# Performance work log

Measured on AMD Instinct MI355X. Metric: run time of the kernel, lower is better.

The kernel has to match this reference:

```python
import jax, jax.numpy as jnp
import numpy as np

N = 50000       # population nodes
E = 1_600_000   # edges per edge type
F_IN = 2000     # flattened individual-graph embedding (100*20)
D = 20          # hidden channels per TransformerConv head (heads=1)
NEG_SLOPE = 0.01
BN_EPS = 1e-5


def setup_inputs() -> dict:
    key = jax.random.key(0)
    ks = jax.random.split(key, 24)
    features = jax.random.normal(ks[0], (N, F_IN), jnp.float32)
    same_index = jax.random.randint(ks[1], (2, E), 0, N, dtype=jnp.int64)
    diff_index = jax.random.randint(ks[2], (2, E), 0, N, dtype=jnp.int64)
    s0 = 1.0 / np.sqrt(F_IN)
    s1 = 1.0 / np.sqrt(D)
    # layer 0 conv params, stacked over the 2 edge types (same, diff)
    W0q = jax.random.normal(ks[3], (2, F_IN, D), jnp.float32) * s0
    W0k = jax.random.normal(ks[4], (2, F_IN, D), jnp.float32) * s0
    W0v = jax.random.normal(ks[5], (2, F_IN, D), jnp.float32) * s0
    W0s = jax.random.normal(ks[6], (2, F_IN, D), jnp.float32) * s0
    b0q = jnp.zeros((2, D)); b0k = jnp.zeros((2, D))
    b0v = jnp.zeros((2, D)); b0s = jnp.zeros((2, D))
    # layers 1..3 conv params: [layer, edge_type, D, D]
    Wq = jax.random.normal(ks[7], (3, 2, D, D), jnp.float32) * s1
    Wk = jax.random.normal(ks[8], (3, 2, D, D), jnp.float32) * s1
    Wv = jax.random.normal(ks[9], (3, 2, D, D), jnp.float32) * s1
    Ws = jax.random.normal(ks[10], (3, 2, D, D), jnp.float32) * s1
    bq = jnp.zeros((3, 2, D)); bk = jnp.zeros((3, 2, D))
    bv = jnp.zeros((3, 2, D)); bs = jnp.zeros((3, 2, D))
    w1 = jnp.full((4,), 0.8, jnp.float32)
    w2 = jnp.full((4,), 0.2, jnp.float32)
    bn_gamma = jnp.ones((4, D), jnp.float32)
    bn_beta = jnp.zeros((4, D), jnp.float32)
    Wout = jax.random.normal(ks[11], (4 * D, 2), jnp.float32) / np.sqrt(4 * D)
    bout = jnp.zeros((2,), jnp.float32)
    return dict(features=features, same_index=same_index, diff_index=diff_index,
                W0q=W0q, b0q=b0q, W0k=W0k, b0k=b0k, W0v=W0v, b0v=b0v, W0s=W0s, b0s=b0s,
                Wq=Wq, bq=bq, Wk=Wk, bk=bk, Wv=Wv, bv=bv, Ws=Ws, bs=bs,
                w1=w1, w2=w2, bn_gamma=bn_gamma, bn_beta=bn_beta, Wout=Wout, bout=bout)


def _tconv(x, edge_index, Wq, bq, Wk, bk, Wv, bv, Ws, bs):
    """PyG TransformerConv, heads=1, concat=True, root_weight=True, no edge_attr."""
    src, dst = edge_index[0], edge_index[1]
    q = x @ Wq + bq   # [N, D]
    k = x @ Wk + bk
    v = x @ Wv + bv
    logits = jnp.einsum('ed,ed->e', q[dst], k[src]) / jnp.sqrt(jnp.float32(D))  # [E]
    m = jax.ops.segment_max(logits, dst, num_segments=N)
    m = jnp.where(jnp.isfinite(m), m, jnp.float32(0.0))  # nodes with no in-edges
    e = jnp.exp(logits - m[dst])
    z = jax.ops.segment_sum(e, dst, num_segments=N)
    alpha = e / (z[dst] + 1e-16)  # PyG softmax epsilon
    agg = jax.ops.segment_sum(alpha[:, None] * v[src], dst, num_segments=N)  # [N, D]
    return agg + x @ Ws + bs  # skip (root) connection


def _bn(x, gamma, beta):
    mu = x.mean(axis=0)
    var = x.var(axis=0)
    return (x - mu) * jax.lax.rsqrt(var + BN_EPS) * gamma + beta


def reference(features, same_index, diff_index,
              W0q, b0q, W0k, b0k, W0v, b0v, W0s, b0s,
              Wq, bq, Wk, bk, Wv, bv, Ws, bs,
              w1, w2, bn_gamma, bn_beta, Wout, bout):
    x = features
    fcs = []
    for l in range(4):
        if l == 0:
            p_same = (W0q[0], b0q[0], W0k[0], b0k[0], W0v[0], b0v[0], W0s[0], b0s[0])
            p_diff = (W0q[1], b0q[1], W0k[1], b0k[1], W0v[1], b0v[1], W0s[1], b0s[1])
        else:
            i = l - 1
            p_same = (Wq[i, 0], bq[i, 0], Wk[i, 0], bk[i, 0], Wv[i, 0], bv[i, 0], Ws[i, 0], bs[i, 0])
            p_diff = (Wq[i, 1], bq[i, 1], Wk[i, 1], bk[i, 1], Wv[i, 1], bv[i, 1], Ws[i, 1], bs[i, 1])
        x1 = _tconv(x, same_index, *p_same)
        x2 = _tconv(x, diff_index, *p_diff)
        t = w1[l] + w2[l]
        x = (w1[l] / t) * x1 + (w2[l] / t) * x2
        x = _bn(x, bn_gamma[l], bn_beta[l])
        x = jax.nn.leaky_relu(x, NEG_SLOPE)
        fcs.append(x)
    fc = jnp.concatenate(fcs, axis=-1)  # [N, 80]
    return fc @ Wout + bout  # [N, 2]
```

## Files before the change

kernel.cpp:

```cpp
#include <hip/hip_runtime.h>
#include <math.h>

#define N_NODES 50000
#define E_EDGES 1600000
#define F_IN    2000
#define D       20
#define NCOL    160
#define KPAD    2016
#define NBNP    64

#define INV_SQRT_D 0.22360679774997896f

typedef __bf16 bf16x8 __attribute__((ext_vector_type(8)));
typedef __bf16 bf16x4 __attribute__((ext_vector_type(4)));
typedef float  f32x4  __attribute__((ext_vector_type(4)));


__global__ void pack_kernel(
    const float* __restrict__ W0q, const float* __restrict__ W0k,
    const float* __restrict__ W0v, const float* __restrict__ W0s,
    const float* __restrict__ b0q, const float* __restrict__ b0k,
    const float* __restrict__ b0v, const float* __restrict__ b0s,
    const float* __restrict__ Wq,  const float* __restrict__ Wk,
    const float* __restrict__ Wv,  const float* __restrict__ Ws_,
    const float* __restrict__ bq,  const float* __restrict__ bk,
    const float* __restrict__ bv,  const float* __restrict__ bs_,
    __bf16* __restrict__ B0, float* __restrict__ bias0,
    float* __restrict__ WL, float* __restrict__ biasL,
    float* __restrict__ bnp, int* __restrict__ deg)
{
  long idx = (long)blockIdx.x * blockDim.x + threadIdx.x;
  if (idx < (long)NCOL*KPAD) {
    int col = (int)(idx / KPAD), k = (int)(idx % KPAD);
    int et = col / 80, r = col % 80, mat = r / 20, d = r % 20;
    const float* w = (mat==0)?W0q:(mat==1)?W0s:(mat==2)?W0k:W0v;
    float v = (k < F_IN) ? w[((size_t)et*F_IN + k)*D + d] : 0.f;
    B0[idx] = (__bf16)v;
    return;
  }
  idx -= (long)NCOL*KPAD;
  if (idx < 160) {
    int col = (int)idx;
    int et = col / 80, r = col % 80, mat = r / 20, d = r % 20;
    const float* b = (mat==0)?b0q:(mat==1)?b0s:(mat==2)?b0k:b0v;
    bias0[col] = b[et*D + d];
    return;
  }
  idx -= 160;
  if (idx < 9600) {
    int l = (int)(idx / 3200), rem = (int)(idx % 3200);
    int k = rem / NCOL, col = rem % NCOL;
    int et = col / 80, r = col % 80, mat = r / 20, d = r % 20;
    const float* w = (mat==0)?Wq:(mat==1)?Ws_:(mat==2)?Wk:Wv;
    WL[idx] = w[(((size_t)l*2 + et)*D + k)*D + d];
    return;
  }
  idx -= 9600;
  if (idx < 480) {
    int l = (int)(idx / NCOL), col = (int)(idx % NCOL);
    int et = col / 80, r = col % 80, mat = r / 20, d = r % 20;
    const float* b = (mat==0)?bq:(mat==1)?bs_:(mat==2)?bk:bv;
    biasL[idx] = b[(l*2 + et)*D + d];
    return;
  }
  idx -= 480;
  if (idx < 4*NBNP*40) { bnp[idx] = 0.f; return; }
  idx -= 4*NBNP*40;
  if (idx < 2*N_NODES) { deg[idx] = 0; return; }
}

#define SC_EPT 16
#define SC_CHUNK (256*SC_EPT)

__global__ void hist_kernel(const int* __restrict__ same, const int* __restrict__ diff,
                            int* __restrict__ deg)
{
  const int part  = blockIdx.x & 7;
  const int chunk = blockIdx.x >> 3;
  const int lo = part * (N_NODES/8);
  const int hi = lo + (N_NODES/8);
  const long i0 = (long)chunk * SC_CHUNK + threadIdx.x;
#pragma unroll
  for (int it = 0; it < SC_EPT; ++it) {
    long i = i0 + (long)it*256;
    if (i >= 2L*E_EDGES) break;
    int et = (i >= E_EDGES) ? 1 : 0;
    long e = i - (long)et*E_EDGES;
    const int* ix = et ? diff : same;
    int dst = ix[E_EDGES + e];
    if (dst >= lo && dst < hi)
      atomicAdd(&deg[(size_t)et*N_NODES + dst], 1);
  }
}

__global__ void scan_kernel(const int* __restrict__ deg,
                            int* __restrict__ rowptr0, int* __restrict__ rowptr1,
                            int* __restrict__ next0, int* __restrict__ next1)
{
  const int et = blockIdx.x;
  const int* dg = deg + (size_t)et*N_NODES;
  int* rp = et ? rowptr1 : rowptr0;
  int* np = et ? next1 : next0;
  __shared__ int part[1024];
  const int t = threadIdx.x;
  const int per = (N_NODES + 1023) / 1024;
  const int b = t * per;
  const int e = (b + per < N_NODES) ? (b + per) : N_NODES;
  int s = 0;
  for (int i = b; i < e; i++) s += dg[i];
  part[t] = s;
  __syncthreads();
  for (int o = 1; o < 1024; o <<= 1) {
    int v = (t >= o) ? part[t-o] : 0;
    __syncthreads();
    part[t] += v;
    __syncthreads();
  }
  int run = (t == 0) ? 0 : part[t-1];
  for (int i = b; i < e; i++) {
    rp[i] = run; np[i] = run;
    run += dg[i];
  }
  if (t == 0) rp[N_NODES] = part[1023];
}

__global__ void scatter_kernel(const int* __restrict__ same, const int* __restrict__ diff,
                               int* __restrict__ next0, int* __restrict__ next1,
                               int* __restrict__ adj0, int* __restrict__ adj1)
{
  const int part  = blockIdx.x & 7;
  const int chunk = blockIdx.x >> 3;
  const int lo = part * (N_NODES/8);
  const int hi = lo + (N_NODES/8);
  const long i0 = (long)chunk * SC_CHUNK + threadIdx.x;
#pragma unroll
  for (int it = 0; it < SC_EPT; ++it) {
    long i = i0 + (long)it*256;
    if (i >= 2L*E_EDGES) break;
    int et = (i >= E_EDGES) ? 1 : 0;
    long e = i - (long)et*E_EDGES;
    const int* ix = et ? diff : same;
    int dst = ix[E_EDGES + e];
    if (dst >= lo && dst < hi) {
      int src = ix[e];
      int* np  = et ? next1 : next0;
      int* adj = et ? adj1  : adj0;
      int pos = atomicAdd(&np[dst], 1);
      adj[pos] = src;
    }
  }
}

__launch_bounds__(256)
__global__ void gemm0_mfma(const float* __restrict__ A,
                           const __bf16* __restrict__ Bt,
                           const float* __restrict__ bias,
                           __bf16* __restrict__ QS,
                           __bf16* __restrict__ KV0, __bf16* __restrict__ KV1)
{
  __shared__ __bf16 as[2][64*32];
  const int t    = threadIdx.x;
  const int lane = t & 63;
  const int wid  = t >> 6;
  const int wr   = wid >> 1;
  const int wc   = wid & 1;
  const int rb0  = blockIdx.x * 64;

  const int srow = t >> 2;
  const int skc  = (t & 3) * 8;
  const int arow = rb0 + srow;
  const float* aptr = A + (size_t)arow * F_IN;

  const int lrow = lane & 15;
  const int lkb  = (lane >> 4) * 8;

  f32x4 acc[2][5];
#pragma unroll
  for (int i = 0; i < 2; i++)
#pragma unroll
    for (int j = 0; j < 5; j++) acc[i][j] = (f32x4){0.f,0.f,0.f,0.f};

  auto loadA = [&](int k0, float4& q0, float4& q1) {
    int k = k0 + skc;
    if (arow < N_NODES) {
      if (k + 8 <= F_IN) {
        q0 = *(const float4*)(aptr + k);
        q1 = *(const float4*)(aptr + k + 4);
      } else {
        float tmp[8];
#pragma unroll
        for (int i = 0; i < 8; i++) tmp[i] = (k + i < F_IN) ? aptr[k + i] : 0.f;
        q0 = make_float4(tmp[0],tmp[1],tmp[2],tmp[3]);
        q1 = make_float4(tmp[4],tmp[5],tmp[6],tmp[7]);
      }
    } else {
      q0 = make_float4(0,0,0,0); q1 = q0;
    }
  };
  auto cvtStore = [&](int buf, const float4& q0, const float4& q1) {
    bf16x8 h;
    h[0]=(__bf16)q0.x; h[1]=(__bf16)q0.y; h[2]=(__bf16)q0.z; h[3]=(__bf16)q0.w;
    h[4]=(__bf16)q1.x; h[5]=(__bf16)q1.y; h[6]=(__bf16)q1.z; h[7]=(__bf16)q1.w;
    *(bf16x8*)&as[buf][srow*32 + skc] = h;
  };

  float4 pa0, pa1, pb0, pb1;
  loadA(0,  pa0, pa1);
  loadA(32, pb0, pb1);
  cvtStore(0, pa0, pa1);
  __syncthreads();

  for (int s = 0; s < 63; s++) {
    const int cur = s & 1;
    bf16x8 af[2];
#pragma unroll
    for (int rf = 0; rf < 2; rf++)
      af[rf] = *(bf16x8*)&as[cur][(wr*32 + rf*16 + lrow)*32 + lkb];
    bf16x8 bfr[5];
#pragma unroll
    for (int cf = 0; cf < 5; cf++)
      bfr[cf] = *(const bf16x8*)(Bt + (size_t)(wc*80 + cf*16 + lrow)*KPAD + s*32 + lkb);

    if (s + 1 < 63) cvtStore(cur ^ 1, pb0, pb1);
    if (s + 2 < 63) loadA((s + 2) * 32, pa0, pa1);

#pragma unroll
    for (int rf = 0; rf < 2; rf++)
#pragma unroll
      for (int cf = 0; cf < 5; cf++)
        acc[rf][cf] = __builtin_amdgcn_mfma_f32_16x16x32_bf16(af[rf], bfr[cf], acc[rf][cf], 0, 0, 0);
    __syncthreads();

    float4 t0 = pa0, t1 = pa1;
    pa0 = pb0; pa1 = pb1;
    pb0 = t0;  pb1 = t1;
  }

#pragma unroll
  for (int rf = 0; rf < 2; rf++) {
#pragma unroll
    for (int cf = 0; cf < 5; cf++) {
      int col = wc*80 + cf*16 + lrow;
      int et = col / 80, r = col % 80, mat = r / 20, d = r % 20;
      float bv = bias[col];
      __bf16* kvp = et ? KV1 : KV0;
#pragma unroll
      for (int j = 0; j < 4; j++) {
        int row = rb0 + wr*32 + rf*16 + (lane >> 4)*4 + j;
        if (row < N_NODES) {
          __bf16 val = (__bf16)(acc[rf][cf][j] + bv);
          if (mat < 2) QS[(size_t)row*80 + et*40 + mat*20 + d] = val;
          else         kvp[(size_t)row*64 + (mat-2)*20 + d]   = val;
        }
      }
    }
  }
}

__launch_bounds__(256)
__global__ void proj_small_kernel(const float* __restrict__ xp, const float* __restrict__ bnl,
                                  const float* __restrict__ gam, const float* __restrict__ bet,
                                  const float* __restrict__ W, const float* __restrict__ bias,
                                  __bf16* __restrict__ QS,
                                  __bf16* __restrict__ KV0, __bf16* __restrict__ KV1)
{
  __shared__ float ws[20*160];
  __shared__ float xs[16*20];
  __shared__ float Ac[20], Bc[20];
  const int t = threadIdx.x;
  const int n0 = blockIdx.x * 16;
#pragma unroll
  for (int i = 0; i < 13; i++) {
    int idx = t + i*256;
    if (idx < 3200) ws[idx] = W[idx];
  }
  if (t < 20) {
    float s1 = 0.f, s2 = 0.f;
    for (int s = 0; s < NBNP; s++) { s1 += bnl[s*40 + t]; s2 += bnl[s*40 + 20 + t]; }
    float mu  = s1 * (1.f/N_NODES);
    float var = s2 * (1.f/N_NODES) - mu*mu;
    float a = rsqrtf(var + 1e-5f) * gam[t];
    Ac[t] = a; Bc[t] = bet[t] - mu*a;
  }
  __syncthreads();
#pragma unroll
  for (int i = 0; i < 2; i++) {
    int idx = t + i*256;
    if (idx < 320) {
      int nl = idx / 20, k = idx % 20;
      int n = n0 + nl;
      float x = (n < N_NODES) ? xp[(size_t)n*D + k] : 0.f;
      float y = x*Ac[k] + Bc[k];
      xs[idx] = (y > 0.f) ? y : 0.01f*y;
    }
  }
  __syncthreads();
#pragma unroll
  for (int i = 0; i < 10; i++) {
    int idx = t + i*256;
    int nl = idx / NCOL, col = idx % NCOL;
    int n = n0 + nl;
    if (n < N_NODES) {
      float acc = bias[col];
#pragma unroll
      for (int k = 0; k < 20; k++) acc += xs[nl*20 + k] * ws[k*NCOL + col];
      int et = col / 80, r = col % 80, mat = r / 20, d = r % 20;
      __bf16 val = (__bf16)acc;
      if (mat < 2) QS[(size_t)n*80 + et*40 + mat*20 + d] = val;
      else         (et ? KV1 : KV0)[(size_t)n*64 + (mat-2)*20 + d] = val;
    }
  }
}

__launch_bounds__(256)
__global__ void attn_fused(const int* __restrict__ rp0, const int* __restrict__ adj0,
                           const int* __restrict__ rp1, const int* __restrict__ adj1,
                           const __bf16* __restrict__ QS,
                           const __bf16* __restrict__ KV0, const __bf16* __restrict__ KV1,
                           const float* __restrict__ w1, const float* __restrict__ w2, int l,
                           float* __restrict__ xpre, float* __restrict__ bnp)
{
  const int t    = threadIdx.x;
  const int wv   = t >> 6;
  const int lane = t & 63;
  const int g    = lane >> 4;
  const int sl   = lane & 15;
  const int et   = g & 1;
  const int node = blockIdx.x*8 + wv*2 + (g >> 1);

  const int* rowptr = et ? rp1 : rp0;
  const int* adj    = et ? adj1 : adj0;
  const __bf16* kvb = et ? KV1 : KV0;
  const __bf16* rq  = QS + (size_t)node*80 + et*40;

  float qf[20];
  {
    bf16x8 q0 = *(const bf16x8*)(rq);
    bf16x8 q1 = *(const bf16x8*)(rq + 8);
    bf16x4 q2 = *(const bf16x4*)(rq + 16);
#pragma unroll
    for (int i = 0; i < 8; i++) { qf[i] = (float)q0[i]; qf[8+i] = (float)q1[i]; }
#pragma unroll
    for (int i = 0; i < 4; i++) qf[16+i] = (float)q2[i];
  }

  const int beg = rowptr[node], end = rowptr[node+1];
  float z = 0.f;
  float S[20];
#pragma unroll
  for (int d = 0; d < 20; d++) S[d] = 0.f;

  int i = beg + sl;
  for (; i + 16 < end; i += 32) {
    const int s0 = adj[i], s1 = adj[i+16];
    const __bf16* kva = kvb + (size_t)s0*64;
    const __bf16* kvc = kvb + (size_t)s1*64;
    bf16x8 a0 = *(const bf16x8*)(kva);
    bf16x8 a1 = *(const bf16x8*)(kva + 8);
    bf16x8 a2 = *(const bf16x8*)(kva + 16);
    bf16x8 a3 = *(const bf16x8*)(kva + 24);
    bf16x8 a4 = *(const bf16x8*)(kva + 32);
    bf16x8 b0 = *(const bf16x8*)(kvc);
    bf16x8 b1 = *(const bf16x8*)(kvc + 8);
    bf16x8 b2 = *(const bf16x8*)(kvc + 16);
    bf16x8 b3 = *(const bf16x8*)(kvc + 24);
    bf16x8 b4 = *(const bf16x8*)(kvc + 32);

    float d0 = 0.f, d1 = 0.f;
#pragma unroll
    for (int j = 0; j < 8; j++) { d0 += qf[j]*(float)a0[j];     d1 += qf[j]*(float)b0[j]; }
#pragma unroll
    for (int j = 0; j < 8; j++) { d0 += qf[8+j]*(float)a1[j];   d1 += qf[8+j]*(float)b1[j]; }
#pragma unroll
    for (int j = 0; j < 4; j++) { d0 += qf[16+j]*(float)a2[j];  d1 += qf[16+j]*(float)b2[j]; }
    const float w0 = __expf(fminf(d0*INV_SQRT_D, 80.f));
    const float w1v= __expf(fminf(d1*INV_SQRT_D, 80.f));
    z += w0 + w1v;
#pragma unroll
    for (int d = 0; d < 4; d++) S[d]     += w0*(float)a2[4+d] + w1v*(float)b2[4+d];
#pragma unroll
    for (int d = 0; d < 8; d++) S[4+d]   += w0*(float)a3[d]   + w1v*(float)b3[d];
#pragma unroll
    for (int d = 0; d < 8; d++) S[12+d]  += w0*(float)a4[d]   + w1v*(float)b4[d];
  }
  if (i < end) {
    const int s0 = adj[i];
    const __bf16* kva = kvb + (size_t)s0*64;
    bf16x8 a0 = *(const bf16x8*)(kva);
    bf16x8 a1 = *(const bf16x8*)(kva + 8);
    bf16x8 a2 = *(const bf16x8*)(kva + 16);
    bf16x8 a3 = *(const bf16x8*)(kva + 24);
    bf16x8 a4 = *(const bf16x8*)(kva + 32);
    float d0 = 0.f;
#pragma unroll
    for (int j = 0; j < 8; j++) d0 += qf[j]     * (float)a0[j];
#pragma unroll
    for (int j = 0; j < 8; j++) d0 += qf[8 + j] * (float)a1[j];
#pragma unroll
    for (int j = 0; j < 4; j++) d0 += qf[16 + j]* (float)a2[j];
    const float w0 = __expf(fminf(d0*INV_SQRT_D, 80.f));
    z += w0;
#pragma unroll
    for (int d = 0; d < 4; d++) S[d]     += w0*(float)a2[4+d];
#pragma unroll
    for (int d = 0; d < 8; d++) S[4+d]   += w0*(float)a3[d];
#pragma unroll
    for (int d = 0; d < 8; d++) S[12+d]  += w0*(float)a4[d];
  }

#pragma unroll
  for (int o = 8; o >= 1; o >>= 1) {
    z += __shfl_xor(z, o, 64);
#pragma unroll
    for (int d = 0; d < 20; d++) S[d] += __shfl_xor(S[d], o, 64);
  }

  const float inv = (z > 0.f) ? 1.f/z : 0.f;
  float outv[20];
  {
    bf16x4 s0 = *(const bf16x4*)(rq + 20);
    bf16x8 s1 = *(const bf16x8*)(rq + 24);
    bf16x8 s2 = *(const bf16x8*)(rq + 32);
#pragma unroll
    for (int i2 = 0; i2 < 4; i2++) outv[i2] = S[i2]*inv + (float)s0[i2];
#pragma unroll
    for (int i2 = 0; i2 < 8; i2++) { outv[4+i2]  = S[4+i2]*inv  + (float)s1[i2];
                                     outv[12+i2] = S[12+i2]*inv + (float)s2[i2]; }
  }

  const float wa = w1[l], wb = w2[l];
  const float c0 = wa/(wa+wb), c1 = wb/(wa+wb);
  const float cme = et ? c1 : c0;
  const float cot = et ? c0 : c1;
  float x[20];
#pragma unroll
  for (int d = 0; d < 20; d++) {
    float o2 = __shfl_xor(outv[d], 16, 64);
    x[d] = cme*outv[d] + cot*o2;
  }

  if (et == 0 && sl == 0) {
    float* xo = xpre + (size_t)node*D;
#pragma unroll
    for (int j = 0; j < 5; j++) {
      float4 o4 = make_float4(x[4*j], x[4*j+1], x[4*j+2], x[4*j+3]);
      *(float4*)(xo + 4*j) = o4;
    }
  }

  float v = x[0];
#pragma unroll
  for (int d = 1; d < 16; d++) v = (sl == d) ? x[d] : v;
  float v2 = x[16];
#pragma unroll
  for (int d = 1; d < 4; d++) v2 = (sl == d) ? x[16 + d] : v2;

  float* slot = bnp + (size_t)(node & (NBNP-1))*40;
  if (et == 0) {
    atomicAdd(&slot[sl], v);
    if (sl < 4) atomicAdd(&slot[16 + sl], v2);
  } else {
    atomicAdd(&slot[20 + sl], v*v);
    if (sl < 4) atomicAdd(&slot[36 + sl], v2*v2);
  }
}

__launch_bounds__(256)
__global__ void final_kernel(const float* __restrict__ xpre4, const float* __restrict__ bnp,
                             const float* __restrict__ gam, const float* __restrict__ bet,
                             const float* __restrict__ Wout, const float* __restrict__ bout,
                             float* __restrict__ out)
{
  __shared__ float Ac[80], Bc[80], wlds[160];
  const int t = threadIdx.x;
  if (t < 80) {
    int l = t / 20, d = t % 20;
    const float* b = bnp + l*(NBNP*40);
    float s1 = 0.f, s2 = 0.f;
    for (int s = 0; s < NBNP; s++) { s1 += b[s*40 + d]; s2 += b[s*40 + 20 + d]; }
    float mu  = s1 * (1.f/N_NODES);
    float var = s2 * (1.f/N_NODES) - mu*mu;
    float a = rsqrtf(var + 1e-5f) * gam[t];
    Ac[t] = a; Bc[t] = bet[t] - mu*a;
  }
  if (t < 160) wlds[t] = Wout[t];
  __syncthreads();

  const int n = blockIdx.x*256 + t;
  if (n >= N_NODES) return;
  float a0 = bout[0], a1 = bout[1];
#pragma unroll
  for (int l = 0; l < 4; l++) {
    const float* base = xpre4 + (size_t)l*N_NODES*D + (size_t)n*D;
#pragma unroll
    for (int d = 0; d < D; d++) {
      int idx = l*20 + d;
      float y = base[d]*Ac[idx] + Bc[idx];
      y = (y > 0.f) ? y : 0.01f*y;
      a0 += y * wlds[idx*2 + 0];
      a1 += y * wlds[idx*2 + 1];
    }
  }
  out[n*2+0] = a0;
  out[n*2+1] = a1;
}

extern "C" void kernel_launch(void* const* d_in, const int* in_sizes, int n_in,
                              void* d_out, int out_size, void* d_ws, size_t ws_size,
                              hipStream_t stream)
{
  const float* feat = (const float*)d_in[0];
  const int*   same = (const int*)d_in[1];
  const int*   diff = (const int*)d_in[2];
  const float* W0q = (const float*)d_in[3];
  const float* b0q = (const float*)d_in[4];
  const float* W0k = (const float*)d_in[5];
  const float* b0k = (const float*)d_in[6];
  const float* W0v = (const float*)d_in[7];
  const float* b0v = (const float*)d_in[8];
  const float* W0s = (const float*)d_in[9];
  const float* b0s = (const float*)d_in[10];
  const float* Wq  = (const float*)d_in[11];
  const float* bq  = (const float*)d_in[12];
  const float* Wk  = (const float*)d_in[13];
  const float* bk  = (const float*)d_in[14];
  const float* Wv  = (const float*)d_in[15];
  const float* bv  = (const float*)d_in[16];
  const float* Ws_ = (const float*)d_in[17];
  const float* bs_ = (const float*)d_in[18];
  const float* w1  = (const float*)d_in[19];
  const float* w2  = (const float*)d_in[20];
  const float* gamma = (const float*)d_in[21];
  const float* beta  = (const float*)d_in[22];
  const float* Wout  = (const float*)d_in[23];
  const float* bout  = (const float*)d_in[24];

  float* wsf  = (float*)d_ws;
  __bf16*  QS    = (__bf16*)wsf;
  __bf16*  KV0   = (__bf16*)(wsf + 2000000);
  __bf16*  KV1   = (__bf16*)(wsf + 3600000);
  float*   XPRE4 = wsf + 5200000;
  __bf16*  B0bf  = (__bf16*)(wsf + 9200000);
  float*   BIAS0 = wsf + 9361280;
  float*   WL    = wsf + 9361440;
  float*   BIASL = wsf + 9371040;
  float*   BNP   = wsf + 9371520;
  int*     ib    = (int*)(wsf + 9381760);
  int* DEG  = ib;
  int* RP0  = ib + 100000;
  int* RP1  = ib + 150004;
  int* NX0  = ib + 200008;
  int* NX1  = ib + 250008;
  int* ADJ0 = ib + 300008;
  int* ADJ1 = ib + 1900008;

  const int packN = NCOL*KPAD + 160 + 9600 + 480 + 4*NBNP*40 + 2*N_NODES;
  pack_kernel<<<(packN + 255)/256, 256, 0, stream>>>(
      W0q, W0k, W0v, W0s, b0q, b0k, b0v, b0s,
      Wq, Wk, Wv, Ws_, bq, bk, bv, bs_,
      B0bf, BIAS0, WL, BIASL, BNP, DEG);

  const long nchunk = (2L*E_EDGES + SC_CHUNK - 1) / SC_CHUNK;
  hist_kernel<<<(int)(nchunk*8), 256, 0, stream>>>(same, diff, DEG);
  scan_kernel<<<2, 1024, 0, stream>>>(DEG, RP0, RP1, NX0, NX1);
  scatter_kernel<<<(int)(nchunk*8), 256, 0, stream>>>(same, diff, NX0, NX1, ADJ0, ADJ1);

  for (int l = 0; l < 4; l++) {
    if (l == 0)
      gemm0_mfma<<<(N_NODES + 63)/64, 256, 0, stream>>>(feat, B0bf, BIAS0, QS, KV0, KV1);
    else
      proj_small_kernel<<<(N_NODES + 15)/16, 256, 0, stream>>>(
          XPRE4 + (size_t)(l-1)*N_NODES*D, BNP + (l-1)*(NBNP*40),
          gamma + (l-1)*D, beta + (l-1)*D,
          WL + (size_t)(l-1)*3200, BIASL + (size_t)(l-1)*160, QS, KV0, KV1);

    attn_fused<<<N_NODES/8, 256, 0, stream>>>(
        RP0, ADJ0, RP1, ADJ1, QS, KV0, KV1, w1, w2, l,
        XPRE4 + (size_t)l*N_NODES*D, BNP + l*(NBNP*40));
  }

  final_kernel<<<(N_NODES + 255)/256, 256, 0, stream>>>(
      XPRE4, BNP, gamma, beta, Wout, bout, (float*)d_out);
}
```

Baseline: 977.3 us.

## Load A fragments directly into registers, dropping LDS staging and barriers in gemm0

Restructures the layer-0 GEMM so each wave owns 16 rows and all 160 output columns. A rows are loaded straight from global memory into the MFMA fragment layout and converted to bf16 in registers, with a 3-deep register prefetch. This removes the shared-memory tile, its writes and reads, and the per-step __syncthreads. In exchange each wave now loads all 10 B fragments per step, doubling B traffic per A row, and the A loads are 32-byte strided chunks per lane instead of the previous cooperative layout.

```diff
diff --git a/kernel.cpp b/kernel.cpp
--- a/kernel.cpp
+++ b/kernel.cpp
@@ -158,100 +158,68 @@
                            __bf16* __restrict__ QS,
                            __bf16* __restrict__ KV0, __bf16* __restrict__ KV1)
 {
-  __shared__ __bf16 as[2][64*32];
   const int t    = threadIdx.x;
   const int lane = t & 63;
   const int wid  = t >> 6;
-  const int wr   = wid >> 1;
-  const int wc   = wid & 1;
   const int rb0  = blockIdx.x * 64;
-
-  const int srow = t >> 2;
-  const int skc  = (t & 3) * 8;
-  const int arow = rb0 + srow;
-  const float* aptr = A + (size_t)arow * F_IN;
-
   const int lrow = lane & 15;
   const int lkb  = (lane >> 4) * 8;
 
-  f32x4 acc[2][5];
-#pragma unroll
-  for (int i = 0; i < 2; i++)
-#pragma unroll
-    for (int j = 0; j < 5; j++) acc[i][j] = (f32x4){0.f,0.f,0.f,0.f};
-
-  auto loadA = [&](int k0, float4& q0, float4& q1) {
-    int k = k0 + skc;
-    if (arow < N_NODES) {
-      if (k + 8 <= F_IN) {
-        q0 = *(const float4*)(aptr + k);
-        q1 = *(const float4*)(aptr + k + 4);
-      } else {
-        float tmp[8];
-#pragma unroll
-        for (int i = 0; i < 8; i++) tmp[i] = (k + i < F_IN) ? aptr[k + i] : 0.f;
-        q0 = make_float4(tmp[0],tmp[1],tmp[2],tmp[3]);
-        q1 = make_float4(tmp[4],tmp[5],tmp[6],tmp[7]);
-      }
+  const int arow = rb0 + wid*16 + lrow;
+  const bool rowok = arow < N_NODES;
+  const float* aptr = A + (size_t)arow * F_IN;
+
+  f32x4 acc[10];
+#pragma unroll
+  for (int cf = 0; cf < 10; cf++) acc[cf] = (f32x4){0.f,0.f,0.f,0.f};
+
+  auto loadA = [&](int s, float4& q0, float4& q1) {
+    int k = s*32 + lkb;
+    if (rowok && k + 8 <= F_IN) {
+      q0 = *(const float4*)(aptr + k);
+      q1 = *(const float4*)(aptr + k + 4);
     } else {
       q0 = make_float4(0,0,0,0); q1 = q0;
     }
   };
-  auto cvtStore = [&](int buf, const float4& q0, const float4& q1) {
-    bf16x8 h;
-    h[0]=(__bf16)q0.x; h[1]=(__bf16)q0.y; h[2]=(__bf16)q0.z; h[3]=(__bf16)q0.w;
-    h[4]=(__bf16)q1.x; h[5]=(__bf16)q1.y; h[6]=(__bf16)q1.z; h[7]=(__bf16)q1.w;
-    *(bf16x8*)&as[buf][srow*32 + skc] = h;
-  };
-
-  float4 pa0, pa1, pb0, pb1;
-  loadA(0,  pa0, pa1);
-  loadA(32, pb0, pb1);
-  cvtStore(0, pa0, pa1);
-  __syncthreads();
+
+  float4 p0a, p0b, p1a, p1b, p2a, p2b;
+  loadA(0, p0a, p0b);
+  loadA(1, p1a, p1b);
+  loadA(2, p2a, p2b);
 
   for (int s = 0; s < 63; s++) {
-    const int cur = s & 1;
-    bf16x8 af[2];
-#pragma unroll
-    for (int rf = 0; rf < 2; rf++)
-      af[rf] = *(bf16x8*)&as[cur][(wr*32 + rf*16 + lrow)*32 + lkb];
-    bf16x8 bfr[5];
-#pragma unroll
-    for (int cf = 0; cf < 5; cf++)
-      bfr[cf] = *(const bf16x8*)(Bt + (size_t)(wc*80 + cf*16 + lrow)*KPAD + s*32 + lkb);
-
-    if (s + 1 < 63) cvtStore(cur ^ 1, pb0, pb1);
-    if (s + 2 < 63) loadA((s + 2) * 32, pa0, pa1);
-
-#pragma unroll
-    for (int rf = 0; rf < 2; rf++)
-#pragma unroll
-      for (int cf = 0; cf < 5; cf++)
-        acc[rf][cf] = __builtin_amdgcn_mfma_f32_16x16x32_bf16(af[rf], bfr[cf], acc[rf][cf], 0, 0, 0);
-    __syncthreads();
-
-    float4 t0 = pa0, t1 = pa1;
-    pa0 = pb0; pa1 = pb1;
-    pb0 = t0;  pb1 = t1;
-  }
-
-#pragma unroll
-  for (int rf = 0; rf < 2; rf++) {
-#pragma unroll
-    for (int cf = 0; cf < 5; cf++) {
-      int col = wc*80 + cf*16 + lrow;
-      int et = col / 80, r = col % 80, mat = r / 20, d = r % 20;
-      float bv = bias[col];
-      __bf16* kvp = et ? KV1 : KV0;
-#pragma unroll
-      for (int j = 0; j < 4; j++) {
-        int row = rb0 + wr*32 + rf*16 + (lane >> 4)*4 + j;
-        if (row < N_NODES) {
-          __bf16 val = (__bf16)(acc[rf][cf][j] + bv);
-          if (mat < 2) QS[(size_t)row*80 + et*40 + mat*20 + d] = val;
-          else         kvp[(size_t)row*64 + (mat-2)*20 + d]   = val;
-        }
+    bf16x8 bfr[10];
+#pragma unroll
+    for (int cf = 0; cf < 10; cf++)
+      bfr[cf] = *(const bf16x8*)(Bt + (size_t)(cf*16 + lrow)*KPAD + s*32 + lkb);
+
+    bf16x8 af;
+    af[0]=(__bf16)p0a.x; af[1]=(__bf16)p0a.y; af[2]=(__bf16)p0a.z; af[3]=(__bf16)p0a.w;
+    af[4]=(__bf16)p0b.x; af[5]=(__bf16)p0b.y; af[6]=(__bf16)p0b.z; af[7]=(__bf16)p0b.w;
+
+    p0a = p1a; p0b = p1b;
+    p1a = p2a; p1b = p2b;
+    if (s + 3 < 63) loadA(s + 3, p2a, p2b);
+
+#pragma unroll
+    for (int cf = 0; cf < 10; cf++)
+      acc[cf] = __builtin_amdgcn_mfma_f32_16x16x32_bf16(af, bfr[cf], acc[cf], 0, 0, 0);
+  }
+
+#pragma unroll
+  for (int cf = 0; cf < 10; cf++) {
+    int col = cf*16 + lrow;
+    int et = col / 80, r = col % 80, mat = r / 20, d = r % 20;
+    float bv = bias[col];
+    __bf16* kvp = et ? KV1 : KV0;
+#pragma unroll
+    for (int j = 0; j < 4; j++) {
+      int row = rb0 + wid*16 + (lane >> 4)*4 + j;
+      if (row < N_NODES) {
+        __bf16 val = (__bf16)(acc[cf][j] + bv);
+        if (mat < 2) QS[(size_t)row*80 + et*40 + mat*20 + d] = val;
+        else         kvp[(size_t)row*64 + (mat-2)*20 + d]   = val;
       }
     }
   }
```

New measurement: 1.181 ms. 20.9% more time.

## Deepen gemm0 K-tile to 128 with padded LDS stride and fewer syncs

Applied to the files above, without the earlier changes.

The layer-0 feature GEMM now loads a 128-wide K slab per stage (8 float4 per thread) instead of 32. It runs 16 pipeline steps with four MFMA sub-steps each, so there are far fewer barriers and more loads in flight per thread. The LDS row stride is padded to 136 to avoid bank conflicts, and the packed weight matrix is padded to K=2048, with workspace offsets shifted to match. The cost is more registers and LDS per block, which may lower occupancy, plus some wasted MFMA work on the zero-padded tail.

```diff
diff --git a/kernel.cpp b/kernel.cpp
--- a/kernel.cpp
+++ b/kernel.cpp
@@ -6,7 +6,9 @@
 #define F_IN    2000
 #define D       20
 #define NCOL    160
-#define KPAD    2016
+#define KPAD2   2048
+#define NSTEP   16
+#define LSTR2   136
 #define NBNP    64
 
 #define INV_SQRT_D 0.22360679774997896f
@@ -30,15 +32,15 @@
     float* __restrict__ bnp, int* __restrict__ deg)
 {
   long idx = (long)blockIdx.x * blockDim.x + threadIdx.x;
-  if (idx < (long)NCOL*KPAD) {
-    int col = (int)(idx / KPAD), k = (int)(idx % KPAD);
+  if (idx < (long)NCOL*KPAD2) {
+    int col = (int)(idx / KPAD2), k = (int)(idx % KPAD2);
     int et = col / 80, r = col % 80, mat = r / 20, d = r % 20;
     const float* w = (mat==0)?W0q:(mat==1)?W0s:(mat==2)?W0k:W0v;
     float v = (k < F_IN) ? w[((size_t)et*F_IN + k)*D + d] : 0.f;
     B0[idx] = (__bf16)v;
     return;
   }
-  idx -= (long)NCOL*KPAD;
+  idx -= (long)NCOL*KPAD2;
   if (idx < 160) {
     int col = (int)idx;
     int et = col / 80, r = col % 80, mat = r / 20, d = r % 20;
@@ -158,7 +160,7 @@
                            __bf16* __restrict__ QS,
                            __bf16* __restrict__ KV0, __bf16* __restrict__ KV1)
 {
-  __shared__ __bf16 as[2][64*32];
+  __shared__ __bf16 as[2][64*LSTR2];
   const int t    = threadIdx.x;
   const int lane = t & 63;
   const int wid  = t >> 6;
@@ -167,7 +169,7 @@
   const int rb0  = blockIdx.x * 64;
 
   const int srow = t >> 2;
-  const int skc  = (t & 3) * 8;
+  const int scol = (t & 3) * 32;
   const int arow = rb0 + srow;
   const float* aptr = A + (size_t)arow * F_IN;
 
@@ -180,60 +182,54 @@
 #pragma unroll
     for (int j = 0; j < 5; j++) acc[i][j] = (f32x4){0.f,0.f,0.f,0.f};
 
-  auto loadA = [&](int k0, float4& q0, float4& q1) {
-    int k = k0 + skc;
-    if (arow < N_NODES) {
-      if (k + 8 <= F_IN) {
-        q0 = *(const float4*)(aptr + k);
-        q1 = *(const float4*)(aptr + k + 4);
-      } else {
-        float tmp[8];
-#pragma unroll
-        for (int i = 0; i < 8; i++) tmp[i] = (k + i < F_IN) ? aptr[k + i] : 0.f;
-        q0 = make_float4(tmp[0],tmp[1],tmp[2],tmp[3]);
-        q1 = make_float4(tmp[4],tmp[5],tmp[6],tmp[7]);
-      }
-    } else {
-      q0 = make_float4(0,0,0,0); q1 = q0;
+  float4 P[8];
+  auto loadA = [&](int s) {
+    const int k0 = s*128 + scol;
+#pragma unroll
+    for (int j = 0; j < 8; j++) {
+      int k = k0 + j*4;
+      P[j] = (arow < N_NODES && k + 4 <= F_IN) ? *(const float4*)(aptr + k)
+                                               : make_float4(0.f,0.f,0.f,0.f);
     }
   };
-  auto cvtStore = [&](int buf, const float4& q0, const float4& q1) {
-    bf16x8 h;
-    h[0]=(__bf16)q0.x; h[1]=(__bf16)q0.y; h[2]=(__bf16)q0.z; h[3]=(__bf16)q0.w;
-    h[4]=(__bf16)q1.x; h[5]=(__bf16)q1.y; h[6]=(__bf16)q1.z; h[7]=(__bf16)q1.w;
-    *(bf16x8*)&as[buf][srow*32 + skc] = h;
+  auto cvtStore = [&](int buf) {
+#pragma unroll
+    for (int j = 0; j < 4; j++) {
+      bf16x8 h;
+      h[0]=(__bf16)P[2*j].x;   h[1]=(__bf16)P[2*j].y;
+      h[2]=(__bf16)P[2*j].z;   h[3]=(__bf16)P[2*j].w;
+      h[4]=(__bf16)P[2*j+1].x; h[5]=(__bf16)P[2*j+1].y;
+      h[6]=(__bf16)P[2*j+1].z; h[7]=(__bf16)P[2*j+1].w;
+      *(bf16x8*)&as[buf][srow*LSTR2 + scol + j*8] = h;
+    }
   };
 
-  float4 pa0, pa1, pb0, pb1;
-  loadA(0,  pa0, pa1);
-  loadA(32, pb0, pb1);
-  cvtStore(0, pa0, pa1);
+  loadA(0); cvtStore(0);
+  loadA(1);
   __syncthreads();
 
-  for (int s = 0; s < 63; s++) {
+  for (int s = 0; s < NSTEP; s++) {
     const int cur = s & 1;
-    bf16x8 af[2];
-#pragma unroll
-    for (int rf = 0; rf < 2; rf++)
-      af[rf] = *(bf16x8*)&as[cur][(wr*32 + rf*16 + lrow)*32 + lkb];
-    bf16x8 bfr[5];
-#pragma unroll
-    for (int cf = 0; cf < 5; cf++)
-      bfr[cf] = *(const bf16x8*)(Bt + (size_t)(wc*80 + cf*16 + lrow)*KPAD + s*32 + lkb);
-
-    if (s + 1 < 63) cvtStore(cur ^ 1, pb0, pb1);
-    if (s + 2 < 63) loadA((s + 2) * 32, pa0, pa1);
-
-#pragma unroll
-    for (int rf = 0; rf < 2; rf++)
+    if (s + 1 < NSTEP) cvtStore(cur ^ 1);
+    if (s + 2 < NSTEP) loadA(s + 2);
+
+#pragma unroll
+    for (int kk = 0; kk < 4; kk++) {
+      bf16x8 af[2];
+#pragma unroll
+      for (int rf = 0; rf < 2; rf++)
+        af[rf] = *(bf16x8*)&as[cur][(wr*32 + rf*16 + lrow)*LSTR2 + kk*32 + lkb];
+      bf16x8 bfr[5];
 #pragma unroll
       for (int cf = 0; cf < 5; cf++)
-        acc[rf][cf] = __builtin_amdgcn_mfma_f32_16x16x32_bf16(af[rf], bfr[cf], acc[rf][cf], 0, 0, 0);
+        bfr[cf] = *(const bf16x8*)(Bt + (size_t)(wc*80 + cf*16 + lrow)*KPAD2 + s*128 + kk*32 + lkb);
+#pragma unroll
+      for (int rf = 0; rf < 2; rf++)
+#pragma unroll
+        for (int cf = 0; cf < 5; cf++)
+          acc[rf][cf] = __builtin_amdgcn_mfma_f32_16x16x32_bf16(af[rf], bfr[cf], acc[rf][cf], 0, 0, 0);
+    }
     __syncthreads();
-
-    float4 t0 = pa0, t1 = pa1;
-    pa0 = pb0; pa1 = pb1;
-    pb0 = t0;  pb1 = t1;
   }
 
 #pragma unroll
@@ -541,11 +537,11 @@
   __bf16*  KV1   = (__bf16*)(wsf + 3600000);
   float*   XPRE4 = wsf + 5200000;
   __bf16*  B0bf  = (__bf16*)(wsf + 9200000);
-  float*   BIAS0 = wsf + 9361280;
-  float*   WL    = wsf + 9361440;
-  float*   BIASL = wsf + 9371040;
-  float*   BNP   = wsf + 9371520;
-  int*     ib    = (int*)(wsf + 9381760);
+  float*   BIAS0 = wsf + 9363840;
+  float*   WL    = wsf + 9364000;
+  float*   BIASL = wsf + 9373600;
+  float*   BNP   = wsf + 9374080;
+  int*     ib    = (int*)(wsf + 9384320);
   int* DEG  = ib;
   int* RP0  = ib + 100000;
   int* RP1  = ib + 150004;
@@ -554,7 +550,7 @@
   int* ADJ0 = ib + 300008;
   int* ADJ1 = ib + 1900008;
 
-  const int packN = NCOL*KPAD + 160 + 9600 + 480 + 4*NBNP*40 + 2*N_NODES;
+  const int packN = NCOL*KPAD2 + 160 + 9600 + 480 + 4*NBNP*40 + 2*N_NODES;
   pack_kernel<<<(packN + 255)/256, 256, 0, stream>>>(
       W0q, W0k, W0v, W0s, b0q, b0k, b0v, b0s,
       Wq, Wk, Wv, Ws_, bq, bk, bv, bs_,
```

Result: slower. 1.062 ms (+8.6%).
